# Kernel optimization log

Measured on AMD Instinct MI355X. Metric: run time of the kernel, lower is better.

The kernel has to match this reference:

```python
import jax, jax.numpy as jnp
import numpy as np


def setup_inputs() -> dict:
    key = jax.random.key(0)
    ks = jax.random.split(key, 7)
    B, T, C, D = 8, 2048, 1024, 128
    x = jax.random.normal(ks[0], (B, T, C), dtype=jnp.float32)
    # torch nn.Linear weights are [out_features, in_features]
    s = 1.0 / np.sqrt(C)
    Wq = jax.random.normal(ks[1], (D, C), dtype=jnp.float32) * s
    bq = jax.random.normal(ks[2], (D,), dtype=jnp.float32) * s
    Wk = jax.random.normal(ks[3], (D, C), dtype=jnp.float32) * s
    bk = jax.random.normal(ks[4], (D,), dtype=jnp.float32) * s
    Wv = jax.random.normal(ks[5], (D, C), dtype=jnp.float32) * s
    bv = jax.random.normal(ks[6], (D,), dtype=jnp.float32) * s
    return {"x": x, "Wq": Wq, "bq": bq, "Wk": Wk, "bk": bk, "Wv": Wv, "bv": bv}


def reference(x, Wq, bq, Wk, bk, Wv, bv):
    B, T, C = x.shape
    q = jnp.einsum('btc,dc->btd', x, Wq) + bq  # [B,T,D]
    k = jnp.einsum('btc,dc->btd', x, Wk) + bk
    v = jnp.einsum('btc,dc->btd', x, Wv) + bv
    scores = jnp.einsum('btd,bsd->bts', q, k)  # [B,T,T]
    causal = jnp.tril(jnp.ones((T, T), dtype=bool))
    masked = jnp.where(causal, scores, -jnp.inf)
    # NOTE: original scales by sqrt(key.weight.shape[-1]) == sqrt(emb_dim), AFTER masking
    scale = jnp.asarray(C, dtype=x.dtype) ** 0.5
    attn = jax.nn.softmax(masked / scale, axis=-1)
    return jnp.einsum('bts,bsd->btd', attn, v)
```

## Files before the change

kernel.cpp:

```cpp
#include <hip/hip_runtime.h>
#include <hip/hip_bf16.h>
#include <math.h>

typedef __bf16 bf16_t;
typedef __bf16 bf16x4 __attribute__((ext_vector_type(4)));
typedef __bf16 bf16x8 __attribute__((ext_vector_type(8)));
typedef float  f32x4  __attribute__((ext_vector_type(4)));
typedef float  f32x16 __attribute__((ext_vector_type(16)));
typedef int    v2i    __attribute__((ext_vector_type(2)));

static constexpr int Bz = 8, Tt = 2048, Cc = 1024, Dd = 128;
static constexpr int Mm = Bz * Tt;
static constexpr int NT128 = Tt / 128;

__device__ __forceinline__ bf16x8 lds_read8(const char* base, int byte) {
    return *(const bf16x8*)(base + byte);
}

__device__ __forceinline__ bf16x8 cvt8(float4 a, float4 b) {
    bf16x8 r;
    r[0] = (bf16_t)a.x; r[1] = (bf16_t)a.y; r[2] = (bf16_t)a.z; r[3] = (bf16_t)a.w;
    r[4] = (bf16_t)b.x; r[5] = (bf16_t)b.y; r[6] = (bf16_t)b.z; r[7] = (bf16_t)b.w;
    return r;
}

__device__ __forceinline__ unsigned cvtpk(float lo, float hi) {
    unsigned r;
    asm("v_cvt_pk_bf16_f32 %0, %1, %2" : "=v"(r) : "v"(lo), "v"(hi));
    return r;
}

typedef const __attribute__((address_space(1))) unsigned int* as1_u32p;
typedef __attribute__((address_space(3))) unsigned int* as3_u32p;

__device__ __forceinline__ void gload_lds16(const bf16_t* g, bf16_t* l) {
    __builtin_amdgcn_global_load_lds((as1_u32p)(const void*)g, (as3_u32p)(void*)l, 16, 0, 0);
}

__global__ __launch_bounds__(256) void wcvt_kernel(
    const float* __restrict__ Wq, const float* __restrict__ Wk,
    const float* __restrict__ Wv, bf16_t* __restrict__ Wp)
{
    int g = (blockIdx.x * 256 + threadIdx.x) * 4;
    int n = g >> 10;
    int k = g & 1023;
    int sel = n >> 7;
    const float* W = (sel == 0) ? Wq : (sel == 1) ? Wk : Wv;
    float4 f = *(const float4*)(W + (size_t)(n & 127) * 1024 + k);
    bf16x4 o; o[0] = (bf16_t)f.x; o[1] = (bf16_t)f.y; o[2] = (bf16_t)f.z; o[3] = (bf16_t)f.w;
    int ktile = k >> 6, kk = (k >> 5) & 1, hi = (k >> 3) & 3, e = k & 7;
    int ng = n >> 4, cg = ng / 12, ngl = ng % 12, lo = n & 15;
    size_t addr = (size_t)(((((ktile * 2 + cg) * 12 + ngl) * 2 + kk) * 4 + hi) * 16 + lo) * 8 + e;
    *(bf16x4*)(Wp + addr) = o;
}

__global__ __launch_bounds__(512, 4) void qkv_fused(
    const float* __restrict__ x, const bf16_t* __restrict__ Wp,
    const float* __restrict__ bq, const float* __restrict__ bk, const float* __restrict__ bv,
    bf16_t* __restrict__ qo, bf16_t* __restrict__ ko, bf16_t* __restrict__ vTo)
{
    const int m0  = blockIdx.x * 64;
    const int cg  = blockIdx.y;
    const int tid = threadIdx.x;
    const int lane = tid & 63;
    const int wv  = tid >> 6;
    const int wr  = wv >> 2;
    const int cw  = wv & 3;
    const int lo  = lane & 15;
    const int hi  = lane >> 4;

    __shared__ bf16_t Wl[2][12 * 2 * 512];
    __shared__ bf16_t Xs[2][64 * 64];

    f32x4 zero4 = {0.f, 0.f, 0.f, 0.f};
    f32x4 acc[2][3];
    #pragma unroll
    for (int i = 0; i < 2; i++)
        #pragma unroll
        for (int j = 0; j < 3; j++) acc[i][j] = zero4;

    const int xrow = tid >> 3;
    const int xcol = (tid & 7) * 8;

    float4 fx[2];
    auto load_x = [&](int t) {
        const float4* s = (const float4*)(x + (size_t)(m0 + xrow) * Cc + t * 64 + xcol);
        fx[0] = s[0]; fx[1] = s[1];
    };
    auto write_x = [&](int buf) {
        int byte = (xrow * 128 + xcol * 2) ^ ((xrow & 7) << 4);
        *(bf16x8*)((char*)Xs[buf] + byte) = cvt8(fx[0], fx[1]);
    };
    auto stage_W = [&](int buf, int t) {
        const bf16_t* base = Wp + (size_t)(t * 2 + cg) * 12288;
        #pragma unroll
        for (int i = 0; i < 3; i++) {
            int c = i * 8 + wv;
            gload_lds16(base + c * 512 + lane * 8, Wl[buf] + c * 512);
        }
    };

    stage_W(0, 0); load_x(0); write_x(0);
    __syncthreads();

    for (int t = 0; t < 16; t++) {
        const int buf = t & 1;
        const bool more = (t < 15);
        if (more) { stage_W(buf ^ 1, t + 1); load_x(t + 1); }
        #pragma unroll
        for (int kk = 0; kk < 2; kk++) {
            int r0 = wr * 32 + lo;
            int r1 = wr * 32 + 16 + lo;
            bf16x8 af0 = lds_read8((char*)Xs[buf], (r0 * 128 + kk * 64 + hi * 16) ^ ((r0 & 7) << 4));
            bf16x8 af1 = lds_read8((char*)Xs[buf], (r1 * 128 + kk * 64 + hi * 16) ^ ((r1 & 7) << 4));
            #pragma unroll
            for (int j = 0; j < 3; j++) {
                int ngl = cw * 3 + j;
                bf16x8 bf = *(const bf16x8*)(Wl[buf] + (ngl * 2 + kk) * 512 + lane * 8);
                acc[0][j] = __builtin_amdgcn_mfma_f32_16x16x32_bf16(af0, bf, acc[0][j], 0, 0, 0);
                acc[1][j] = __builtin_amdgcn_mfma_f32_16x16x32_bf16(af1, bf, acc[1][j], 0, 0, 0);
            }
        }
        if (more) write_x(buf ^ 1);
        __syncthreads();
    }

    #pragma unroll
    for (int j = 0; j < 3; j++) {
        int n = cg * 192 + cw * 48 + j * 16 + lo;
        int tsel = n >> 7, d = n & 127;
        const float* bp = (tsel == 0) ? bq : (tsel == 1) ? bk : bv;
        float bb = bp[d];
        #pragma unroll
        for (int i = 0; i < 2; i++)
            #pragma unroll
            for (int r = 0; r < 4; r++) {
                int m = m0 + wr * 32 + i * 16 + hi * 4 + r;
                float v = acc[i][j][r] + bb;
                if (tsel == 0)      qo[(size_t)m * Dd + d] = (bf16_t)v;
                else if (tsel == 1) ko[(size_t)m * Dd + d] = (bf16_t)v;
                else                vTo[(size_t)d * Mm + m] = (bf16_t)v;
            }
    }
}

__global__ __launch_bounds__(256, 2) void attn_kernel(
    const bf16_t* __restrict__ qi, const bf16_t* __restrict__ ki,
    const bf16_t* __restrict__ vTi,
    float* __restrict__ Opart, float* __restrict__ Mpart, float* __restrict__ Lpart,
    int nsplit)
{
    const int g   = blockIdx.x;
    const int per = nsplit * 8;
    const int qt  = (NT128 - 1) - g / per;
    const int rem = g % per;
    const int s   = rem >> 3;
    const int b   = rem & 7;
    const int nt  = 2 * qt + 2;
    const int t_lo = (s * nt) / nsplit;
    const int t_hi = ((s + 1) * nt) / nsplit;

    const int q0   = qt * 128;
    const int tid  = threadIdx.x;
    const int lane = tid & 63;
    const int w    = tid >> 6;
    const int rq   = lane & 31;
    const int dh   = lane >> 5;

    float* Ob = Opart + ((size_t)s * Mm + (size_t)b * Tt + q0) * Dd;
    float* Mb = Mpart + (size_t)s * Mm + (size_t)b * Tt + q0;
    float* Lb = Lpart + (size_t)s * Mm + (size_t)b * Tt + q0;

    if (t_lo >= t_hi) {
        float4 z = {0.f, 0.f, 0.f, 0.f};
        #pragma unroll
        for (int i = 0; i < 16; i++)
            ((float4*)Ob)[i * 256 + tid] = z;
        if (tid < 128) { Mb[tid] = -INFINITY; Lb[tid] = 0.f; }
        return;
    }

    __shared__ __align__(16) char smem[65536];

    const float SCALE = 1.4426950408889634f / 32.0f;
    const int qg = q0 + w * 32 + rq;
    const int qwmax = q0 + w * 32 + 31;

    bf16x8 qf[8];
    {
        const bf16_t* qrow = qi + (size_t)(b * Tt + qg) * Dd;
        #pragma unroll
        for (int ks = 0; ks < 8; ks++)
            qf[ks] = *(const bf16x8*)(qrow + ks * 16 + dh * 8);
    }

    f32x16 accO[4];
    #pragma unroll
    for (int ds = 0; ds < 4; ds++)
        #pragma unroll
        for (int e = 0; e < 16; e++) accO[ds][e] = 0.f;
    float mrun = -INFINITY, lrun = 0.f;

    const int krow = tid >> 2;
    const int kcol = (tid & 3) * 32;
    const int vrow = tid >> 1;
    const int vcol = (tid & 1) * 32;

    bf16x8 kr[4], vr[4];
    auto load_kv = [&](int t) {
        const int kv0 = t * 64;
        const bf16_t* ksrc = ki + (size_t)(b * Tt + kv0 + krow) * Dd + kcol;
        #pragma unroll
        for (int i = 0; i < 4; i++) kr[i] = *(const bf16x8*)(ksrc + i * 8);
        const bf16_t* vsrc = vTi + (size_t)vrow * Mm + (b * Tt + kv0 + vcol);
        #pragma unroll
        for (int i = 0; i < 4; i++) vr[i] = *(const bf16x8*)(vsrc + i * 8);
    };
    auto write_kv = [&](int buf) {
        char* Ksb = smem + buf * 16384;
        char* Vsb = smem + 32768 + buf * 16384;
        #pragma unroll
        for (int i = 0; i < 4; i++) {
            int byte = (krow * 256 + (kcol + i * 8) * 2) ^ ((krow & 15) << 4);
            *(bf16x8*)(Ksb + byte) = kr[i];
        }
        const int vlr = vrow & 63;
        const int vlc = (vrow >> 6) * 64 + vcol;
        #pragma unroll
        for (int i = 0; i < 4; i++) {
            int byte = (vlr * 256 + (vlc + i * 8) * 2) ^ ((vlr & 15) << 4);
            *(bf16x8*)(Vsb + byte) = vr[i];
        }
    };

    load_kv(t_lo);
    write_kv(0);
    int buf = 0;

    for (int t = t_lo; t < t_hi; t++) {
        const int kv0 = t * 64;
        const bool more = (t + 1 < t_hi);
        __syncthreads();
        if (more) load_kv(t + 1);

        if (kv0 <= qwmax) {
            const char* Ksb = smem + buf * 16384;
            const char* Vsb = smem + 32768 + buf * 16384;

            f32x16 accS0, accS1;
            #pragma unroll
            for (int e = 0; e < 16; e++) { accS0[e] = 0.f; accS1[e] = 0.f; }
            #pragma unroll
            for (int ks = 0; ks < 8; ks++) {
                int colb = (ks * 16 + dh * 8) * 2;
                bf16x8 kf0 = lds_read8(Ksb, ((rq)      * 256 + colb) ^ ((rq & 15) << 4));
                bf16x8 kf1 = lds_read8(Ksb, ((32 + rq) * 256 + colb) ^ ((rq & 15) << 4));
                accS0 = __builtin_amdgcn_mfma_f32_32x32x16_bf16(kf0, qf[ks], accS0, 0, 0, 0);
                accS1 = __builtin_amdgcn_mfma_f32_32x32x16_bf16(kf1, qf[ks], accS1, 0, 0, 0);
            }

            float pl[32];
            #pragma unroll
            for (int e = 0; e < 16; e++) {
                pl[e]      = accS0[e] * SCALE;
                pl[16 + e] = accS1[e] * SCALE;
            }
            if (kv0 + 63 > qg) {
                #pragma unroll
                for (int e = 0; e < 16; e++) {
                    int kg = kv0 + 8 * (e >> 2) + (e & 3) + 4 * dh;
                    if (kg > qg)      pl[e]      = -INFINITY;
                    if (kg + 32 > qg) pl[16 + e] = -INFINITY;
                }
            }

            float mt = pl[0];
            #pragma unroll
            for (int e = 1; e < 32; e++) mt = fmaxf(mt, pl[e]);
            mt = fmaxf(mt, __shfl_xor(mt, 32, 64));
            float mnew = fmaxf(mrun, mt);
            float muse = (mnew == -INFINITY) ? 0.f : mnew;
            float alpha = exp2f(mrun - muse);
            mrun = mnew;
            float ps = 0.f;
            #pragma unroll
            for (int e = 0; e < 32; e++) {
                float pv = exp2f(pl[e] - muse);
                pl[e] = pv;
                ps += pv;
            }
            lrun = alpha * lrun + ps;
            #pragma unroll
            for (int ds = 0; ds < 4; ds++)
                #pragma unroll
                for (int e = 0; e < 16; e++) accO[ds][e] *= alpha;

            unsigned u0[8], u1[8];
            #pragma unroll
            for (int gg = 0; gg < 8; gg++) {
                u0[gg] = cvtpk(pl[4 * gg + 0], pl[4 * gg + 1]);
                u1[gg] = cvtpk(pl[4 * gg + 2], pl[4 * gg + 3]);
            }
            bf16x8 pa[4];
            #pragma unroll
            for (int ks = 0; ks < 4; ks++) {
                v2i rA = __builtin_amdgcn_permlane32_swap((int)u0[2 * ks], (int)u0[2 * ks + 1], false, false);
                v2i rB = __builtin_amdgcn_permlane32_swap((int)u1[2 * ks], (int)u1[2 * ks + 1], false, false);
                union { unsigned wd[4]; bf16x8 v; } pu;
                pu.wd[0] = (unsigned)rA[0];
                pu.wd[1] = (unsigned)rB[0];
                pu.wd[2] = (unsigned)rA[1];
                pu.wd[3] = (unsigned)rB[1];
                pa[ks] = pu.v;
            }

            #pragma unroll
            for (int ds = 0; ds < 4; ds++) {
                int row  = (ds & 1) * 32 + rq;
                int cb   = (ds >> 1) * 64;
                #pragma unroll
                for (int ks = 0; ks < 4; ks++) {
                    int colb = (cb + ks * 16 + dh * 8) * 2;
                    bf16x8 vf = lds_read8(Vsb, (row * 256 + colb) ^ ((row & 15) << 4));
                    accO[ds] = __builtin_amdgcn_mfma_f32_32x32x16_bf16(vf, pa[ks], accO[ds], 0, 0, 0);
                }
            }
        }

        __syncthreads();
        if (more) write_kv(buf ^ 1);
        buf ^= 1;
    }

    __syncthreads();

    lrun += __shfl_xor(lrun, 32, 64);

    char* slab = smem + w * 8192;
    #pragma unroll
    for (int half = 0; half < 2; half++) {
        #pragma unroll
        for (int dsl = 0; dsl < 2; dsl++) {
            #pragma unroll
            for (int e = 0; e < 16; e++) {
                int d = 8 * (e >> 2) + (e & 3) + 4 * dh + 32 * dsl;
                int byte = (rq * 256 + d * 4) ^ ((rq & 15) << 4);
                *(float*)(slab + byte) = accO[half * 2 + dsl][e];
            }
        }
        __builtin_amdgcn_s_waitcnt(0);
        #pragma unroll
        for (int i = 0; i < 8; i++) {
            int dd = 32 * dh + 4 * i;
            int byte = (rq * 256 + dd * 4) ^ ((rq & 15) << 4);
            float4 val = *(float4*)(slab + byte);
            *(float4*)(Ob + (size_t)(w * 32 + rq) * Dd + half * 64 + dd) = val;
        }
        __builtin_amdgcn_s_waitcnt(0);
    }

    if (lane < 32) {
        Mb[w * 32 + rq] = mrun;
        Lb[w * 32 + rq] = lrun;
    }
}

__global__ __launch_bounds__(256) void combine_kernel(
    const float* __restrict__ Opart, const float* __restrict__ Mpart,
    const float* __restrict__ Lpart, float* __restrict__ out, int nsplit)
{
    int t   = blockIdx.x * 256 + threadIdx.x;
    int row = t >> 5;
    int dq  = (t & 31) << 2;
    float M = -INFINITY;
    for (int s = 0; s < nsplit; s++)
        M = fmaxf(M, Mpart[(size_t)s * Mm + row]);
    float L = 0.f;
    float o0 = 0.f, o1 = 0.f, o2 = 0.f, o3 = 0.f;
    for (int s = 0; s < nsplit; s++) {
        float ms = Mpart[(size_t)s * Mm + row];
        float ws = (ms == -INFINITY) ? 0.f : exp2f(ms - M);
        L += ws * Lpart[(size_t)s * Mm + row];
        float4 p = *(const float4*)(Opart + ((size_t)s * Mm + row) * Dd + dq);
        o0 += ws * p.x; o1 += ws * p.y; o2 += ws * p.z; o3 += ws * p.w;
    }
    float inv = 1.0f / L;
    float4 r; r.x = o0 * inv; r.y = o1 * inv; r.z = o2 * inv; r.w = o3 * inv;
    *(float4*)(out + (size_t)row * Dd + dq) = r;
}

extern "C" void kernel_launch(void* const* d_in, const int* in_sizes, int n_in,
                              void* d_out, int out_size, void* d_ws, size_t ws_size,
                              hipStream_t stream)
{
    const float* x  = (const float*)d_in[0];
    const float* Wq = (const float*)d_in[1];
    const float* bq = (const float*)d_in[2];
    const float* Wk = (const float*)d_in[3];
    const float* bk = (const float*)d_in[4];
    const float* Wv = (const float*)d_in[5];
    const float* bv = (const float*)d_in[6];
    float* out = (float*)d_out;

    bf16_t* qb = (bf16_t*)d_ws;
    bf16_t* kb = qb + (size_t)Mm * Dd;
    bf16_t* vT = kb + (size_t)Mm * Dd;
    bf16_t* Wp = vT + (size_t)Mm * Dd;
    char* p = (char*)(Wp + (size_t)384 * Cc);

    auto need = [&](int ns) {
        return (size_t)3 * Mm * Dd * 2 + (size_t)384 * Cc * 2
             + (size_t)ns * Mm * Dd * 4 + (size_t)ns * Mm * 8;
    };
    int nsplit = 4;
    while (nsplit > 1 && need(nsplit) > ws_size) nsplit >>= 1;

    float* Opart = (float*)p;
    float* Mpart = (float*)(p + (size_t)nsplit * Mm * Dd * 4);
    float* Lpart = Mpart + (size_t)nsplit * Mm;

    wcvt_kernel<<<dim3(384), 256, 0, stream>>>(Wq, Wk, Wv, Wp);
    qkv_fused<<<dim3(256, 2), 512, 0, stream>>>(x, Wp, bq, bk, bv, qb, kb, vT);
    attn_kernel<<<dim3(NT128 * nsplit * Bz), 256, 0, stream>>>(qb, kb, vT, Opart, Mpart, Lpart, nsplit);
    combine_kernel<<<dim3(Mm * 32 / 256), 256, 0, stream>>>(Opart, Mpart, Lpart, out, nsplit);
}
```

Measured before the change: 71.41 us.

## Split KV range across wave pairs in-block and drop separate combine kernel

Attention blocks now cover 64 query rows each, with two wave pairs splitting that tile's KV range in half. Each pair keeps its own single-buffered K/V LDS slab, and the partial results are merged in shared memory before the final output is written. This removes the global Opart/Mpart/Lpart partial buffers and the combine kernel launch, so the fp32 partial traffic goes away. In exchange the grid shrinks to 256 blocks at one block per CU, loses double buffering (two barriers per step), and the unequal causal tiles may leave work imbalanced.

```diff
diff --git a/kernel.cpp b/kernel.cpp
--- a/kernel.cpp
+++ b/kernel.cpp
@@ -11,7 +11,6 @@
 
 static constexpr int Bz = 8, Tt = 2048, Cc = 1024, Dd = 128;
 static constexpr int Mm = Bz * Tt;
-static constexpr int NT128 = Tt / 128;
 
 __device__ __forceinline__ bf16x8 lds_read8(const char* base, int byte) {
     return *(const bf16x8*)(base + byte);
@@ -144,47 +143,36 @@
     }
 }
 
-__global__ __launch_bounds__(256, 2) void attn_kernel(
+__global__ __launch_bounds__(256, 1) void attn_kernel(
     const bf16_t* __restrict__ qi, const bf16_t* __restrict__ ki,
-    const bf16_t* __restrict__ vTi,
-    float* __restrict__ Opart, float* __restrict__ Mpart, float* __restrict__ Lpart,
-    int nsplit)
+    const bf16_t* __restrict__ vTi, float* __restrict__ out)
 {
-    const int g   = blockIdx.x;
-    const int per = nsplit * 8;
-    const int qt  = (NT128 - 1) - g / per;
-    const int rem = g % per;
-    const int s   = rem >> 3;
-    const int b   = rem & 7;
-    const int nt  = 2 * qt + 2;
-    const int t_lo = (s * nt) / nsplit;
-    const int t_hi = ((s + 1) * nt) / nsplit;
-
-    const int q0   = qt * 128;
+    const int g  = blockIdx.x;
+    const int qt = g >> 3;
+    const int b  = g & 7;
+    const int nt = qt + 1;
+    const int h  = (nt + 1) >> 1;
+    const int S  = h;
+
     const int tid  = threadIdx.x;
     const int lane = tid & 63;
     const int w    = tid >> 6;
+    const int qw   = w >> 1;
+    const int sv   = w & 1;
     const int rq   = lane & 31;
     const int dh   = lane >> 5;
 
-    float* Ob = Opart + ((size_t)s * Mm + (size_t)b * Tt + q0) * Dd;
-    float* Mb = Mpart + (size_t)s * Mm + (size_t)b * Tt + q0;
-    float* Lb = Lpart + (size_t)s * Mm + (size_t)b * Tt + q0;
-
-    if (t_lo >= t_hi) {
-        float4 z = {0.f, 0.f, 0.f, 0.f};
-        #pragma unroll
-        for (int i = 0; i < 16; i++)
-            ((float4*)Ob)[i * 256 + tid] = z;
-        if (tid < 128) { Mb[tid] = -INFINITY; Lb[tid] = 0.f; }
-        return;
-    }
+    const int base = sv ? h : 0;
+    const int lim  = sv ? nt : h;
+
+    const int q0 = qt * 64;
+    const int qg = q0 + qw * 32 + rq;
 
     __shared__ __align__(16) char smem[65536];
+    char* Ksb = smem + sv * 32768;
+    char* Vsb = Ksb + 16384;
 
     const float SCALE = 1.4426950408889634f / 32.0f;
-    const int qg = q0 + w * 32 + rq;
-    const int qwmax = q0 + w * 32 + 31;
 
     bf16x8 qf[8];
     {
@@ -201,51 +189,47 @@
         for (int e = 0; e < 16; e++) accO[ds][e] = 0.f;
     float mrun = -INFINITY, lrun = 0.f;
 
-    const int krow = tid >> 2;
-    const int kcol = (tid & 3) * 32;
-    const int vrow = tid >> 1;
-    const int vcol = (tid & 1) * 32;
-
-    bf16x8 kr[4], vr[4];
+    const int gl   = qw * 64 + lane;
+    const int krow = gl >> 1;
+    const int kcol = (gl & 1) * 64;
+    const int vd   = gl;
+    const int vlr  = vd & 63;
+    const int vcb  = (vd >> 6) * 64;
+
+    bf16x8 kr[8], vr[8];
     auto load_kv = [&](int t) {
         const int kv0 = t * 64;
         const bf16_t* ksrc = ki + (size_t)(b * Tt + kv0 + krow) * Dd + kcol;
         #pragma unroll
-        for (int i = 0; i < 4; i++) kr[i] = *(const bf16x8*)(ksrc + i * 8);
-        const bf16_t* vsrc = vTi + (size_t)vrow * Mm + (b * Tt + kv0 + vcol);
-        #pragma unroll
-        for (int i = 0; i < 4; i++) vr[i] = *(const bf16x8*)(vsrc + i * 8);
-    };
-    auto write_kv = [&](int buf) {
-        char* Ksb = smem + buf * 16384;
-        char* Vsb = smem + 32768 + buf * 16384;
-        #pragma unroll
-        for (int i = 0; i < 4; i++) {
+        for (int i = 0; i < 8; i++) kr[i] = *(const bf16x8*)(ksrc + i * 8);
+        const bf16_t* vsrc = vTi + (size_t)vd * Mm + b * Tt + kv0;
+        #pragma unroll
+        for (int i = 0; i < 8; i++) vr[i] = *(const bf16x8*)(vsrc + i * 8);
+    };
+    auto write_kv = [&]() {
+        #pragma unroll
+        for (int i = 0; i < 8; i++) {
             int byte = (krow * 256 + (kcol + i * 8) * 2) ^ ((krow & 15) << 4);
             *(bf16x8*)(Ksb + byte) = kr[i];
         }
-        const int vlr = vrow & 63;
-        const int vlc = (vrow >> 6) * 64 + vcol;
-        #pragma unroll
-        for (int i = 0; i < 4; i++) {
-            int byte = (vlr * 256 + (vlc + i * 8) * 2) ^ ((vlr & 15) << 4);
+        #pragma unroll
+        for (int i = 0; i < 8; i++) {
+            int byte = (vlr * 256 + (vcb + i * 8) * 2) ^ ((vlr & 15) << 4);
             *(bf16x8*)(Vsb + byte) = vr[i];
         }
     };
 
-    load_kv(t_lo);
-    write_kv(0);
-    int buf = 0;
-
-    for (int t = t_lo; t < t_hi; t++) {
-        const int kv0 = t * 64;
-        const bool more = (t + 1 < t_hi);
-        __syncthreads();
-        if (more) load_kv(t + 1);
-
-        if (kv0 <= qwmax) {
-            const char* Ksb = smem + buf * 16384;
-            const char* Vsb = smem + 32768 + buf * 16384;
+    if (base < lim) { load_kv(base); write_kv(); }
+    __syncthreads();
+
+    for (int step = 0; step < S; step++) {
+        const int t = base + step;
+        const bool act  = t < lim;
+        const bool morea = (t + 1) < lim;
+        if (morea) load_kv(t + 1);
+
+        if (act) {
+            const int kv0 = t * 64;
 
             f32x16 accS0, accS1;
             #pragma unroll
@@ -316,8 +300,8 @@
 
             #pragma unroll
             for (int ds = 0; ds < 4; ds++) {
-                int row  = (ds & 1) * 32 + rq;
-                int cb   = (ds >> 1) * 64;
+                int row = (ds & 1) * 32 + rq;
+                int cb  = (ds >> 1) * 64;
                 #pragma unroll
                 for (int ks = 0; ks < 4; ks++) {
                     int colb = (cb + ks * 16 + dh * 8) * 2;
@@ -328,65 +312,61 @@
         }
 
         __syncthreads();
-        if (more) write_kv(buf ^ 1);
-        buf ^= 1;
-    }
-
+        if (morea) write_kv();
+        __syncthreads();
+    }
+
+    lrun += __shfl_xor(lrun, 32, 64);
+
+    if (sv == 1) {
+        float* reg = (float*)(smem + qw * 24576);
+        #pragma unroll
+        for (int ds = 0; ds < 4; ds++)
+            #pragma unroll
+            for (int e = 0; e < 16; e++)
+                reg[(ds * 16 + e) * 64 + lane] = accO[ds][e];
+        reg[4096 + lane] = mrun;
+        reg[4160 + lane] = lrun;
+    }
     __syncthreads();
-
-    lrun += __shfl_xor(lrun, 32, 64);
-
-    char* slab = smem + w * 8192;
-    #pragma unroll
-    for (int half = 0; half < 2; half++) {
-        #pragma unroll
-        for (int dsl = 0; dsl < 2; dsl++) {
-            #pragma unroll
-            for (int e = 0; e < 16; e++) {
-                int d = 8 * (e >> 2) + (e & 3) + 4 * dh + 32 * dsl;
-                int byte = (rq * 256 + d * 4) ^ ((rq & 15) << 4);
-                *(float*)(slab + byte) = accO[half * 2 + dsl][e];
-            }
-        }
-        __builtin_amdgcn_s_waitcnt(0);
-        #pragma unroll
-        for (int i = 0; i < 8; i++) {
-            int dd = 32 * dh + 4 * i;
-            int byte = (rq * 256 + dd * 4) ^ ((rq & 15) << 4);
-            float4 val = *(float4*)(slab + byte);
-            *(float4*)(Ob + (size_t)(w * 32 + rq) * Dd + half * 64 + dd) = val;
-        }
-        __builtin_amdgcn_s_waitcnt(0);
-    }
-
-    if (lane < 32) {
-        Mb[w * 32 + rq] = mrun;
-        Lb[w * 32 + rq] = lrun;
-    }
-}
-
-__global__ __launch_bounds__(256) void combine_kernel(
-    const float* __restrict__ Opart, const float* __restrict__ Mpart,
-    const float* __restrict__ Lpart, float* __restrict__ out, int nsplit)
-{
-    int t   = blockIdx.x * 256 + threadIdx.x;
-    int row = t >> 5;
-    int dq  = (t & 31) << 2;
-    float M = -INFINITY;
-    for (int s = 0; s < nsplit; s++)
-        M = fmaxf(M, Mpart[(size_t)s * Mm + row]);
-    float L = 0.f;
-    float o0 = 0.f, o1 = 0.f, o2 = 0.f, o3 = 0.f;
-    for (int s = 0; s < nsplit; s++) {
-        float ms = Mpart[(size_t)s * Mm + row];
-        float ws = (ms == -INFINITY) ? 0.f : exp2f(ms - M);
-        L += ws * Lpart[(size_t)s * Mm + row];
-        float4 p = *(const float4*)(Opart + ((size_t)s * Mm + row) * Dd + dq);
-        o0 += ws * p.x; o1 += ws * p.y; o2 += ws * p.z; o3 += ws * p.w;
-    }
-    float inv = 1.0f / L;
-    float4 r; r.x = o0 * inv; r.y = o1 * inv; r.z = o2 * inv; r.w = o3 * inv;
-    *(float4*)(out + (size_t)row * Dd + dq) = r;
+    if (sv == 0) {
+        const float* reg = (const float*)(smem + qw * 24576);
+        float m1 = reg[4096 + lane];
+        float l1 = reg[4160 + lane];
+        float m  = fmaxf(mrun, m1);
+        float a0 = exp2f(mrun - m);
+        float a1 = (m1 == -INFINITY) ? 0.f : exp2f(m1 - m);
+        float l  = lrun * a0 + l1 * a1;
+        float inv = 1.0f / l;
+        #pragma unroll
+        for (int ds = 0; ds < 4; ds++)
+            #pragma unroll
+            for (int e = 0; e < 16; e++)
+                accO[ds][e] = (accO[ds][e] * a0 + reg[(ds * 16 + e) * 64 + lane] * a1) * inv;
+
+        char* slab = smem + 49152 + qw * 8192;
+        #pragma unroll
+        for (int half = 0; half < 2; half++) {
+            #pragma unroll
+            for (int dsl = 0; dsl < 2; dsl++) {
+                #pragma unroll
+                for (int e = 0; e < 16; e++) {
+                    int d = 8 * (e >> 2) + (e & 3) + 4 * dh + 32 * dsl;
+                    int byte = (rq * 256 + d * 4) ^ ((rq & 15) << 4);
+                    *(float*)(slab + byte) = accO[half * 2 + dsl][e];
+                }
+            }
+            __builtin_amdgcn_s_waitcnt(0);
+            #pragma unroll
+            for (int i = 0; i < 8; i++) {
+                int dd = 32 * dh + 4 * i;
+                int byte = (rq * 256 + dd * 4) ^ ((rq & 15) << 4);
+                float4 val = *(float4*)(slab + byte);
+                *(float4*)(out + (size_t)(b * Tt + q0 + qw * 32 + rq) * Dd + half * 64 + dd) = val;
+            }
+            __builtin_amdgcn_s_waitcnt(0);
+        }
+    }
 }
 
 extern "C" void kernel_launch(void* const* d_in, const int* in_sizes, int n_in,
@@ -406,21 +386,8 @@
     bf16_t* kb = qb + (size_t)Mm * Dd;
     bf16_t* vT = kb + (size_t)Mm * Dd;
     bf16_t* Wp = vT + (size_t)Mm * Dd;
-    char* p = (char*)(Wp + (size_t)384 * Cc);
-
-    auto need = [&](int ns) {
-        return (size_t)3 * Mm * Dd * 2 + (size_t)384 * Cc * 2
-             + (size_t)ns * Mm * Dd * 4 + (size_t)ns * Mm * 8;
-    };
-    int nsplit = 4;
-    while (nsplit > 1 && need(nsplit) > ws_size) nsplit >>= 1;
-
-    float* Opart = (float*)p;
-    float* Mpart = (float*)(p + (size_t)nsplit * Mm * Dd * 4);
-    float* Lpart = Mpart + (size_t)nsplit * Mm;
 
     wcvt_kernel<<<dim3(384), 256, 0, stream>>>(Wq, Wk, Wv, Wp);
     qkv_fused<<<dim3(256, 2), 512, 0, stream>>>(x, Wp, bq, bk, bv, qb, kb, vT);
-    attn_kernel<<<dim3(NT128 * nsplit * Bz), 256, 0, stream>>>(qb, kb, vT, Opart, Mpart, Lpart, nsplit);
-    combine_kernel<<<dim3(Mm * 32 / 256), 256, 0, stream>>>(Opart, Mpart, Lpart, out, nsplit);
-}
+    attn_kernel<<<dim3(256), 256, 0, stream>>>(qb, kb, vT, out);
+}
```

New measurement: 107.1 us. 49.9% more time.
